# Optimization experiments

Measured on AMD Instinct MI355X. Metric: run time of the kernel, lower is better.

The kernel has to match this reference:

```python
import jax, jax.numpy as jnp
import numpy as np

HEADS = 8
DIM_HEAD = 64
SCALE = DIM_HEAD ** -0.5


def setup_inputs() -> dict:
    key = jax.random.key(0)
    ks = jax.random.split(key, 6)
    b, n, dim, inner = 8, 1024, 512, HEADS * DIM_HEAD
    return {
        "x": jax.random.normal(ks[0], (b, n, dim), jnp.float32),
        "y": jax.random.normal(ks[1], (b, n, dim), jnp.float32),
        "wq": jax.random.normal(ks[2], (dim, inner), jnp.float32) * 0.02,
        "wkv": jax.random.normal(ks[3], (dim, 2 * inner), jnp.float32) * 0.02,
        "wout": jax.random.normal(ks[4], (inner, dim), jnp.float32) * 0.02,
        "bout": jnp.zeros((dim,), jnp.float32),
    }


def _split_heads(t):
    # [b, n, h*d] -> [b, h, n, d]
    b, n, hd = t.shape
    return t.reshape(b, n, HEADS, DIM_HEAD).transpose(0, 2, 1, 3)


def _merge_heads(t):
    # [b, h, n, d] -> [b, n, h*d]
    b, h, n, d = t.shape
    return t.transpose(0, 2, 1, 3).reshape(b, n, h * d)


def _cross_attn(q_in, kv_in, wq, wkv, wout, bout):
    # queries from q_in, keys/values from kv_in; top-(nk//4) masked softmax attention
    nk = kv_in.shape[1]
    q = _split_heads(q_in @ wq)                     # [b,h,nq,d]
    kv = kv_in @ wkv                                # [b,nk,2*inner]
    k, v = jnp.split(kv, 2, axis=-1)
    k, v = _split_heads(k), _split_heads(v)         # [b,h,nk,d]
    dots = jnp.einsum('bhid,bhjd->bhij', q, k) * SCALE  # [b,h,nq,nk]
    kk = max(nk // 4, 1)
    kth = jax.lax.top_k(dots, kk)[0][..., -1:]      # k-th largest per row
    masked = jnp.where(dots >= kth, dots, -jnp.inf)
    attn = jax.nn.softmax(masked, axis=-1)
    out = jnp.einsum('bhij,bhjd->bhid', attn, v)
    return _merge_heads(out) @ wout + bout


def reference(x, y, wq, wkv, wout, bout):
    out_y = _cross_attn(y, x, wq, wkv, wout, bout)  # y attends to x
    out_x = _cross_attn(x, y, wq, wkv, wout, bout)  # x attends to y
    return (out_x, out_y)
```

## Files before the change

kernel.cpp:

```cpp
#include <hip/hip_runtime.h>
#include <hip/hip_bf16.h>

typedef __attribute__((ext_vector_type(8))) short bfx8;
typedef __attribute__((ext_vector_type(4))) float fx4;

__device__ __forceinline__ short f2bf(float f) {
    union { float f; unsigned u; } v; v.f = f;
    unsigned r = v.u + 0x7fffu + ((v.u >> 16) & 1u);
    return (short)(r >> 16);
}
__device__ __forceinline__ float bf2f(short b) {
    union { unsigned u; float f; } v; v.u = ((unsigned)(unsigned short)b) << 16; return v.f;
}

__global__ __launch_bounds__(256) void proj_kernel(
    const float* __restrict__ X, const float* __restrict__ Y,
    const float* __restrict__ wq, const float* __restrict__ wkv,
    short* __restrict__ QpX, short* __restrict__ KpX, short* __restrict__ VbX,
    short* __restrict__ QpY, short* __restrict__ KpY, short* __restrict__ VbY)
{
    const int inp = blockIdx.z;
    const float* A = inp ? Y : X;
    short* Qp = inp ? QpY : QpX;
    short* Kp = inp ? KpY : KpX;
    short* Vb = inp ? VbY : VbX;
    const int mb = blockIdx.x;
    const int nb = blockIdx.y;
    const int tid = threadIdx.x;
    const int lane = tid & 63;
    const int w = tid >> 6, wm = w >> 1, wn = w & 1;
    const int l15 = lane & 15, g8 = (lane >> 4) * 8;

    __shared__ short As[128][72];
    __shared__ short Bs[128][72];

    const float* Bsrc; int ldb, nbase0;
    if (nb < 4) { Bsrc = wq;  ldb = 512;  nbase0 = nb * 128; }
    else        { Bsrc = wkv; ldb = 1024; nbase0 = nb * 128 - 512; }

    fx4 acc[4][4];
    const fx4 z4 = {0.f, 0.f, 0.f, 0.f};
    for (int i = 0; i < 4; i++) for (int j = 0; j < 4; j++) acc[i][j] = z4;

    const int arow = tid >> 1, ahalf = (tid & 1) * 16;
    const int bk = tid >> 3, bnseg = (tid & 7) * 16;

    for (int kb = 0; kb < 512; kb += 32) {
        __syncthreads();
        {
            const float* src = A + (size_t)(mb * 128 + arow) * 512 + kb + ahalf;
            bfx8 h0, h1, l0, l1;
            #pragma unroll
            for (int q = 0; q < 4; q++) {
                float4 v = *(const float4*)(src + q * 4);
                float vv[4] = {v.x, v.y, v.z, v.w};
                #pragma unroll
                for (int c = 0; c < 4; c++) {
                    int idx = q * 4 + c;
                    short h = f2bf(vv[c]);
                    short l = f2bf(vv[c] - bf2f(h));
                    if (idx < 8) { h0[idx] = h; l0[idx] = l; }
                    else         { h1[idx - 8] = h; l1[idx - 8] = l; }
                }
            }
            *(bfx8*)&As[arow][ahalf] = h0;      *(bfx8*)&As[arow][ahalf + 8] = h1;
            *(bfx8*)&As[arow][32 + ahalf] = l0; *(bfx8*)&As[arow][32 + ahalf + 8] = l1;
        }
        {
            const float* src = Bsrc + (size_t)(kb + bk) * ldb + nbase0 + bnseg;
            #pragma unroll
            for (int q = 0; q < 4; q++) {
                float4 v = *(const float4*)(src + q * 4);
                float vv[4] = {v.x, v.y, v.z, v.w};
                #pragma unroll
                for (int c = 0; c < 4; c++) {
                    int n = bnseg + q * 4 + c;
                    short h = f2bf(vv[c]);
                    Bs[n][bk] = h;
                    Bs[n][32 + bk] = f2bf(vv[c] - bf2f(h));
                }
            }
        }
        __syncthreads();
        bfx8 ah[4], al[4], bh[4], bl[4];
        #pragma unroll
        for (int mt = 0; mt < 4; mt++) {
            int r = wm * 64 + mt * 16 + l15;
            ah[mt] = *(bfx8*)&As[r][g8];
            al[mt] = *(bfx8*)&As[r][32 + g8];
        }
        #pragma unroll
        for (int nt = 0; nt < 4; nt++) {
            int r = wn * 64 + nt * 16 + l15;
            bh[nt] = *(bfx8*)&Bs[r][g8];
            bl[nt] = *(bfx8*)&Bs[r][32 + g8];
        }
        #pragma unroll
        for (int mt = 0; mt < 4; mt++)
            #pragma unroll
            for (int nt = 0; nt < 4; nt++) {
                acc[mt][nt] = __builtin_amdgcn_mfma_f32_16x16x32_bf16(ah[mt], bh[nt], acc[mt][nt], 0, 0, 0);
                acc[mt][nt] = __builtin_amdgcn_mfma_f32_16x16x32_bf16(ah[mt], bl[nt], acc[mt][nt], 0, 0, 0);
                acc[mt][nt] = __builtin_amdgcn_mfma_f32_16x16x32_bf16(al[mt], bh[nt], acc[mt][nt], 0, 0, 0);
            }
    }
    #pragma unroll
    for (int mt = 0; mt < 4; mt++)
        #pragma unroll
        for (int nt = 0; nt < 4; nt++)
            #pragma unroll
            for (int r = 0; r < 4; r++) {
                int row = mb * 128 + wm * 64 + mt * 16 + (lane >> 4) * 4 + r;
                int col = nb * 128 + wn * 64 + nt * 16 + l15;
                float v = acc[mt][nt][r];
                int b = row >> 10, n = row & 1023;
                if (col < 512) {
                    v *= 0.125f;
                    int h = col >> 6, d = col & 63;
                    size_t base = ((size_t)(b * 8 + h) * 1024 + n) * 128;
                    short hi = f2bf(v);
                    Qp[base + d] = hi;
                    Qp[base + 64 + d] = f2bf(v - bf2f(hi));
                } else if (col < 1024) {
                    int cc = col - 512;
                    int h = cc >> 6, d = cc & 63;
                    size_t base = ((size_t)(b * 8 + h) * 1024 + n) * 128;
                    short hi = f2bf(v);
                    Kp[base + d] = hi;
                    Kp[base + 64 + d] = f2bf(v - bf2f(hi));
                } else {
                    Vb[(size_t)row * 512 + (col - 1024)] = f2bf(v);
                }
            }
}

__global__ __launch_bounds__(256) void transv_kernel(
    const short* __restrict__ VbX, const short* __restrict__ VbY,
    short* __restrict__ VtX, short* __restrict__ VtY)
{
    const int inp = blockIdx.z;
    const short* Vb = inp ? VbY : VbX;
    short* Vt = inp ? VtY : VtX;
    const int bh = blockIdx.y, b = bh >> 3, h = bh & 7;
    const int nt = blockIdx.x;
    const int tid = threadIdx.x;
    __shared__ short tile[64][66];
    {
        int r = tid >> 2, c0 = (tid & 3) * 16;
        const short* src = Vb + ((size_t)(b * 1024 + nt * 64 + r)) * 512 + h * 64 + c0;
        bfx8 v0 = *(const bfx8*)src;
        bfx8 v1 = *(const bfx8*)(src + 8);
        #pragma unroll
        for (int i = 0; i < 8; i++) { tile[r][c0 + i] = v0[i]; tile[r][c0 + 8 + i] = v1[i]; }
    }
    __syncthreads();
    {
        int d = tid >> 2, n0 = (tid & 3) * 16;
        bfx8 o0, o1;
        #pragma unroll
        for (int i = 0; i < 8; i++) { o0[i] = tile[n0 + i][d]; o1[i] = tile[n0 + 8 + i][d]; }
        short* dst = Vt + ((size_t)(bh * 64 + d)) * 1024 + nt * 64 + n0;
        *(bfx8*)dst = o0;
        *(bfx8*)(dst + 8) = o1;
    }
}

#define PBUF_OFF 0
#define HIST_OFF 65536
#define PMX_OFF  77824
#define PMN_OFF  78336
#define PSUM_OFF 78848
#define RMX_OFF  79360
#define RMN_OFF  79488
#define RT_OFF   79616
#define RB_OFF   79744
#define RN_OFF   79872
#define RC_OFF   80000
#define ATTN_LDS 80128

__global__ __launch_bounds__(512, 4) void attn_kernel(
    const short* __restrict__ QpX, const short* __restrict__ KpX, const short* __restrict__ VtX,
    const short* __restrict__ QpY, const short* __restrict__ KpY, const short* __restrict__ VtY,
    short* __restrict__ inner)
{
    extern __shared__ char smem[];
    unsigned* histU  = (unsigned*)(smem + HIST_OFF);
    float*    candF  = (float*)(smem + HIST_OFF);
    float*    partmx = (float*)(smem + PMX_OFF);
    float*    partmn = (float*)(smem + PMN_OFF);
    float*    partsum= (float*)(smem + PSUM_OFF);
    float*    rowMx  = (float*)(smem + RMX_OFF);
    float*    rowMn  = (float*)(smem + RMN_OFF);
    float*    rowT   = (float*)(smem + RT_OFF);
    int*      rowB   = (int*)(smem + RB_OFF);
    int*      rowNeed= (int*)(smem + RN_OFF);
    int*      rowcnt = (int*)(smem + RC_OFF);

    const int dir = blockIdx.z;
    const short* Qp = dir ? QpY : QpX;
    const short* Kp = dir ? KpX : KpY;
    const short* Vt = dir ? VtX : VtY;
    const int bh = blockIdx.y;
    const int qb = blockIdx.x;
    const int tid = threadIdx.x;
    const int lane = tid & 63;
    const int widx = tid >> 6;
    const int wm = widx >> 2;
    const int ws = widx & 3;
    const int l15 = lane & 15, g = lane >> 4;

    bfx8 qf[2][2];
    {
        const short* qbase = Qp + ((size_t)bh * 1024 + qb * 32 + wm * 16 + l15) * 128;
        #pragma unroll
        for (int ks = 0; ks < 2; ks++)
            #pragma unroll
            for (int p = 0; p < 2; p++)
                qf[ks][p] = *(const bfx8*)(qbase + p * 64 + ks * 32 + g * 8);
    }

    fx4 acc[16];
    {
        const fx4 z4 = {0.f, 0.f, 0.f, 0.f};
        #pragma unroll
        for (int t = 0; t < 16; t++) acc[t] = z4;
        const short* kbase = Kp + ((size_t)bh * 1024 + ws * 256 + l15) * 128 + g * 8;
        #pragma unroll
        for (int t = 0; t < 16; t++) {
            const short* kb = kbase + (size_t)t * 16 * 128;
            bfx8 kh0 = *(const bfx8*)(kb);
            bfx8 kh1 = *(const bfx8*)(kb + 32);
            bfx8 kl0 = *(const bfx8*)(kb + 64);
            bfx8 kl1 = *(const bfx8*)(kb + 96);
            acc[t] = __builtin_amdgcn_mfma_f32_16x16x32_bf16(qf[0][0], kh0, acc[t], 0, 0, 0);
            acc[t] = __builtin_amdgcn_mfma_f32_16x16x32_bf16(qf[0][0], kl0, acc[t], 0, 0, 0);
            acc[t] = __builtin_amdgcn_mfma_f32_16x16x32_bf16(qf[0][1], kh0, acc[t], 0, 0, 0);
            acc[t] = __builtin_amdgcn_mfma_f32_16x16x32_bf16(qf[1][0], kh1, acc[t], 0, 0, 0);
            acc[t] = __builtin_amdgcn_mfma_f32_16x16x32_bf16(qf[1][0], kl1, acc[t], 0, 0, 0);
            acc[t] = __builtin_amdgcn_mfma_f32_16x16x32_bf16(qf[1][1], kh1, acc[t], 0, 0, 0);
        }
    }

    float rmx[4], rmn[4];
    #pragma unroll
    for (int r = 0; r < 4; r++) {
        float a = acc[0][r], b = acc[0][r];
        #pragma unroll
        for (int t = 1; t < 16; t++) { a = fmaxf(a, acc[t][r]); b = fminf(b, acc[t][r]); }
        #pragma unroll
        for (int o = 1; o < 16; o <<= 1) { a = fmaxf(a, __shfl_xor(a, o)); b = fminf(b, __shfl_xor(b, o)); }
        rmx[r] = a; rmn[r] = b;
    }
    if (l15 == 0) {
        #pragma unroll
        for (int r = 0; r < 4; r++) {
            int lrow = wm * 16 + g * 4 + r;
            partmx[lrow * 4 + ws] = rmx[r];
            partmn[lrow * 4 + ws] = rmn[r];
        }
    }
    for (int i = tid; i < 32 * 96; i += 512) histU[i] = 0;
    if (tid < 32) rowcnt[tid] = 0;
    __syncthreads();

    float mxr[4], mnr[4], invr[4];
    #pragma unroll
    for (int r = 0; r < 4; r++) {
        int lrow = wm * 16 + g * 4 + r;
        float a = partmx[lrow * 4 + 0], b = partmn[lrow * 4 + 0];
        #pragma unroll
        for (int j = 1; j < 4; j++) { a = fmaxf(a, partmx[lrow * 4 + j]); b = fminf(b, partmn[lrow * 4 + j]); }
        mxr[r] = a; mnr[r] = b;
        invr[r] = (a - b > 1e-30f) ? 96.0f / (a - b) : 0.0f;
    }
    if (ws == 0 && l15 == 0) {
        #pragma unroll
        for (int r = 0; r < 4; r++) {
            int lrow = wm * 16 + g * 4 + r;
            rowMx[lrow] = mxr[r]; rowMn[lrow] = mnr[r];
        }
    }
    #pragma unroll
    for (int r = 0; r < 4; r++) {
        int lrow = wm * 16 + g * 4 + r;
        #pragma unroll
        for (int t = 0; t < 16; t++) {
            int bin = (int)((acc[t][r] - mnr[r]) * invr[r]);
            bin = bin < 0 ? 0 : (bin > 95 ? 95 : bin);
            atomicAdd(&histU[lrow * 96 + bin], 1u);
        }
    }
    __syncthreads();

    #pragma unroll
    for (int rr = 0; rr < 4; rr++) {
        int row = widx * 4 + rr;
        unsigned c0 = 0, c1 = 0;
        if (lane < 48) { c0 = histU[row * 96 + 2 * lane]; c1 = histU[row * 96 + 2 * lane + 1]; }
        unsigned ts = c0 + c1;
        #pragma unroll
        for (int o = 1; o < 64; o <<= 1) {
            unsigned u = __shfl_down(ts, o);
            if (lane + o < 64) ts += u;
        }
        unsigned ca_lo = ts - c0, ca_hi = ts - c0 - c1;
        bool oklo = (lane < 48) && (ca_lo < 256u) && (ca_lo + c0 >= 256u);
        bool okhi = (lane < 48) && (ca_hi < 256u) && (ca_hi + c1 >= 256u);
        unsigned long long bal = __ballot(oklo || okhi);
        int sl = __ffsll((long long)bal) - 1;
        int myB = oklo ? 2 * lane : 2 * lane + 1;
        int myNeed = 256 - (int)(oklo ? ca_lo : ca_hi);
        int B = __shfl(myB, sl);
        int need = __shfl(myNeed, sl);
        if (lane == 0) {
            float mr = rowMx[row], nr = rowMn[row];
            if (mr - nr < 1e-30f) { rowB[row] = -1; rowT[row] = nr; rowNeed[row] = 1; }
            else { rowB[row] = B; rowNeed[row] = need; }
        }
    }
    __syncthreads();

    #pragma unroll
    for (int r = 0; r < 4; r++) {
        int lrow = wm * 16 + g * 4 + r;
        int B = rowB[lrow];
        #pragma unroll
        for (int t = 0; t < 16; t++) {
            int bin = (int)((acc[t][r] - mnr[r]) * invr[r]);
            bin = bin < 0 ? 0 : (bin > 95 ? 95 : bin);
            if (B >= 0 && bin == B) {
                int idx = atomicAdd(&rowcnt[lrow], 1);
                if (idx < 64) candF[lrow * 64 + idx] = acc[t][r];
            }
        }
    }
    __syncthreads();

    #pragma unroll
    for (int rr = 0; rr < 4; rr++) {
        int row = widx * 4 + rr;
        int B = rowB[row];
        if (B < 0) continue;
        int m = rowcnt[row]; m = m > 64 ? 64 : m;
        int need = rowNeed[row];
        const float* crow = candF + row * 64;
        float v0 = (lane < m) ? crow[lane] : 0.f;
        int cg = 0, ce = 0;
        for (int i = 0; i < m; i++) {
            float c = crow[i];
            cg += (c > v0); ce += (c == v0);
        }
        bool ok = (lane < m) && (cg < need) && (need <= cg + ce);
        unsigned long long bal = __ballot(ok);
        float tt;
        if (bal) tt = __shfl(v0, __ffsll((long long)bal) - 1);
        else     tt = rowMn[row] + (float)B * (rowMx[row] - rowMn[row]) * (1.0f / 96.0f);
        if (lane == 0) rowT[row] = tt;
    }
    __syncthreads();

    #pragma unroll
    for (int r = 0; r < 4; r++) {
        int lrow = wm * 16 + g * 4 + r;
        float tthr = rowT[lrow];
        float s = 0.f;
        unsigned sw = (unsigned)((lrow & 7) << 4);
        #pragma unroll
        for (int t = 0; t < 16; t++) {
            float v = acc[t][r];
            float p = (v >= tthr) ? __expf(v - mxr[r]) : 0.f;
            s += p;
            int col = ws * 256 + t * 16 + l15;
            *(short*)(smem + (size_t)lrow * 2048 + (((unsigned)(col * 2)) ^ sw)) = f2bf(p);
        }
        #pragma unroll
        for (int o = 1; o < 16; o <<= 1) s += __shfl_xor(s, o);
        if (l15 == 0) partsum[lrow * 4 + ws] = s;
    }
    __syncthreads();

    {
        const short* vrow = Vt + ((size_t)bh * 64 + ws * 16 + l15) * 1024;
        const int arow = wm * 16 + l15;
        const unsigned sw = (unsigned)((arow & 7) << 4);
        const char* pbase = smem + (size_t)arow * 2048;
        fx4 acc0 = {0.f, 0.f, 0.f, 0.f}, acc1 = {0.f, 0.f, 0.f, 0.f};
        #pragma unroll
        for (int ks = 0; ks < 32; ks += 2) {
            bfx8 pa0 = *(const bfx8*)(pbase + (((unsigned)(ks * 64 + g * 16)) ^ sw));
            bfx8 vv0 = *(const bfx8*)(vrow + ks * 32 + g * 8);
            bfx8 pa1 = *(const bfx8*)(pbase + (((unsigned)((ks + 1) * 64 + g * 16)) ^ sw));
            bfx8 vv1 = *(const bfx8*)(vrow + (ks + 1) * 32 + g * 8);
            acc0 = __builtin_amdgcn_mfma_f32_16x16x32_bf16(pa0, vv0, acc0, 0, 0, 0);
            acc1 = __builtin_amdgcn_mfma_f32_16x16x32_bf16(pa1, vv1, acc1, 0, 0, 0);
        }
        #pragma unroll
        for (int r = 0; r < 4; r++) {
            int qrow = wm * 16 + g * 4 + r;
            float inv = 1.0f / (partsum[qrow * 4 + 0] + partsum[qrow * 4 + 1] +
                                partsum[qrow * 4 + 2] + partsum[qrow * 4 + 3]);
            float v = (acc0[r] + acc1[r]) * inv;
            size_t orow = (size_t)dir * 8192 + (size_t)(bh >> 3) * 1024 + qb * 32 + qrow;
            inner[orow * 512 + (bh & 7) * 64 + ws * 16 + l15] = f2bf(v);
        }
    }
}

__global__ __launch_bounds__(256) void outproj_kernel(
    const short* __restrict__ inner, const float* __restrict__ wout,
    const float* __restrict__ bout, float* __restrict__ out)
{
    const int mb = blockIdx.x;
    const int nb = blockIdx.y;
    const int tid = threadIdx.x;
    const int lane = tid & 63;
    const int w = tid >> 6, wm = w >> 1, wn = w & 1;
    const int l15 = lane & 15, g8 = (lane >> 4) * 8;

    __shared__ short As[128][40];
    __shared__ short Bs[128][40];

    fx4 acc[4][4];
    const fx4 z4 = {0.f, 0.f, 0.f, 0.f};
    for (int i = 0; i < 4; i++) for (int j = 0; j < 4; j++) acc[i][j] = z4;

    const int arow = tid >> 1, ahalf = (tid & 1) * 16;
    const int bk = tid >> 3, bnseg = (tid & 7) * 16;

    for (int kb = 0; kb < 512; kb += 32) {
        __syncthreads();
        {
            const short* src = inner + (size_t)(mb * 128 + arow) * 512 + kb + ahalf;
            bfx8 v0 = *(const bfx8*)src, v1 = *(const bfx8*)(src + 8);
            *(bfx8*)&As[arow][ahalf] = v0;
            *(bfx8*)&As[arow][ahalf + 8] = v1;
        }
        {
            const float* src = wout + (size_t)(kb + bk) * 512 + nb * 128 + bnseg;
            #pragma unroll
            for (int q = 0; q < 4; q++) {
                float4 v = *(const float4*)(src + q * 4);
                float vv[4] = {v.x, v.y, v.z, v.w};
                #pragma unroll
                for (int c = 0; c < 4; c++) Bs[bnseg + q * 4 + c][bk] = f2bf(vv[c]);
            }
        }
        __syncthreads();
        bfx8 af[4], bf[4];
        #pragma unroll
        for (int mt = 0; mt < 4; mt++) af[mt] = *(bfx8*)&As[wm * 64 + mt * 16 + l15][g8];
        #pragma unroll
        for (int nt = 0; nt < 4; nt++) bf[nt] = *(bfx8*)&Bs[wn * 64 + nt * 16 + l15][g8];
        #pragma unroll
        for (int mt = 0; mt < 4; mt++)
            #pragma unroll
            for (int nt = 0; nt < 4; nt++)
                acc[mt][nt] = __builtin_amdgcn_mfma_f32_16x16x32_bf16(af[mt], bf[nt], acc[mt][nt], 0, 0, 0);
    }
    #pragma unroll
    for (int mt = 0; mt < 4; mt++)
        #pragma unroll
        for (int nt = 0; nt < 4; nt++)
            #pragma unroll
            for (int r = 0; r < 4; r++) {
                int row = mb * 128 + wm * 64 + mt * 16 + (lane >> 4) * 4 + r;
                int col = nb * 128 + wn * 64 + nt * 16 + l15;
                out[(size_t)row * 512 + col] = acc[mt][nt][r] + bout[col];
            }
}

extern "C" void kernel_launch(void* const* d_in, const int* in_sizes, int n_in,
                              void* d_out, int out_size, void* d_ws, size_t ws_size,
                              hipStream_t stream)
{
    const float* x    = (const float*)d_in[0];
    const float* y    = (const float*)d_in[1];
    const float* wq   = (const float*)d_in[2];
    const float* wkv  = (const float*)d_in[3];
    const float* wout = (const float*)d_in[4];
    const float* bout = (const float*)d_in[5];
    float* out = (float*)d_out;

    char* ws = (char*)d_ws;
    size_t off = 0;
    auto alloc = [&](size_t bytes) -> void* {
        void* p = ws + off; off += (bytes + 255) & ~(size_t)255; return p;
    };
    const size_t QP = (size_t)8 * 8 * 1024 * 128 * 2;
    const size_t VB = (size_t)8192 * 512 * 2;
    short* QpX = (short*)alloc(QP);
    short* KpX = (short*)alloc(QP);
    short* QpY = (short*)alloc(QP);
    short* KpY = (short*)alloc(QP);
    short* VbX = (short*)alloc(VB);
    short* VbY = (short*)alloc(VB);
    short* VtX = (short*)alloc(VB);
    short* VtY = (short*)alloc(VB);
    short* inner = (short*)alloc((size_t)2 * 8192 * 512 * 2);
    if (off > ws_size) return;

    proj_kernel<<<dim3(64, 12, 2), 256, 0, stream>>>(x, y, wq, wkv, QpX, KpX, VbX, QpY, KpY, VbY);
    transv_kernel<<<dim3(16, 64, 2), 256, 0, stream>>>(VbX, VbY, VtX, VtY);
    (void)hipFuncSetAttribute((const void*)attn_kernel,
                              hipFuncAttributeMaxDynamicSharedMemorySize, ATTN_LDS);
    attn_kernel<<<dim3(32, 64, 2), 512, ATTN_LDS, stream>>>(QpX, KpX, VtX, QpY, KpY, VtY, inner);
    outproj_kernel<<<dim3(128, 4, 1), 256, 0, stream>>>(inner, wout, bout, out);
}
```

Before: 836.9 us.

## Halve attention query tile to 16 rows, split keys over 8 waves

The attention kernel now handles 16 query rows per block instead of 32. The 8 waves each cover 128 keys, and the PV product is split across two key halves whose partial results are reduced through LDS. LDS use drops from about 80KB to 45KB and per-wave accumulator registers halve, which should allow more resident blocks and more latency hiding. K-fragment loads are also software-prefetched one tile ahead. In exchange, each K/V tile is reloaded for twice as many blocks, and an extra barrier plus partial-sum exchange is added.

Result: faster. 800.3 us (-4.4%).

```diff
diff --git a/kernel.cpp b/kernel.cpp
--- a/kernel.cpp
+++ b/kernel.cpp
@@ -165,18 +165,19 @@
     }
 }
 
-#define PBUF_OFF 0
-#define HIST_OFF 65536
-#define PMX_OFF  77824
-#define PMN_OFF  78336
-#define PSUM_OFF 78848
-#define RMX_OFF  79360
-#define RMN_OFF  79488
-#define RT_OFF   79616
-#define RB_OFF   79744
-#define RN_OFF   79872
-#define RC_OFF   80000
-#define ATTN_LDS 80128
+#define PBUF_BYTES 32768
+#define HIST_OFF   32768
+#define PMX_OFF    38912
+#define PMN_OFF    39424
+#define PSUM_OFF   39936
+#define RMX_OFF    40448
+#define RMN_OFF    40512
+#define RT_OFF     40576
+#define RB_OFF     40640
+#define RN_OFF     40704
+#define RC_OFF     40768
+#define PVP_OFF    40832
+#define ATTN_LDS   44928
 
 __global__ __launch_bounds__(512, 4) void attn_kernel(
     const short* __restrict__ QpX, const short* __restrict__ KpX, const short* __restrict__ VtX,
@@ -195,6 +196,7 @@
     int*      rowB   = (int*)(smem + RB_OFF);
     int*      rowNeed= (int*)(smem + RN_OFF);
     int*      rowcnt = (int*)(smem + RC_OFF);
+    float*    psumPV = (float*)(smem + PVP_OFF);
 
     const int dir = blockIdx.z;
     const short* Qp = dir ? QpY : QpX;
@@ -204,14 +206,12 @@
     const int qb = blockIdx.x;
     const int tid = threadIdx.x;
     const int lane = tid & 63;
-    const int widx = tid >> 6;
-    const int wm = widx >> 2;
-    const int ws = widx & 3;
+    const int w = tid >> 6;
     const int l15 = lane & 15, g = lane >> 4;
 
     bfx8 qf[2][2];
     {
-        const short* qbase = Qp + ((size_t)bh * 1024 + qb * 32 + wm * 16 + l15) * 128;
+        const short* qbase = Qp + ((size_t)bh * 1024 + qb * 16 + l15) * 128;
         #pragma unroll
         for (int ks = 0; ks < 2; ks++)
             #pragma unroll
@@ -219,72 +219,69 @@
                 qf[ks][p] = *(const bfx8*)(qbase + p * 64 + ks * 32 + g * 8);
     }
 
-    fx4 acc[16];
+    fx4 acc[8];
     {
         const fx4 z4 = {0.f, 0.f, 0.f, 0.f};
         #pragma unroll
-        for (int t = 0; t < 16; t++) acc[t] = z4;
-        const short* kbase = Kp + ((size_t)bh * 1024 + ws * 256 + l15) * 128 + g * 8;
-        #pragma unroll
-        for (int t = 0; t < 16; t++) {
-            const short* kb = kbase + (size_t)t * 16 * 128;
-            bfx8 kh0 = *(const bfx8*)(kb);
-            bfx8 kh1 = *(const bfx8*)(kb + 32);
-            bfx8 kl0 = *(const bfx8*)(kb + 64);
-            bfx8 kl1 = *(const bfx8*)(kb + 96);
+        for (int t = 0; t < 8; t++) acc[t] = z4;
+        const short* kbase = Kp + ((size_t)bh * 1024 + w * 128 + l15) * 128 + g * 8;
+        bfx8 kh0 = *(const bfx8*)(kbase);
+        bfx8 kh1 = *(const bfx8*)(kbase + 32);
+        bfx8 kl0 = *(const bfx8*)(kbase + 64);
+        bfx8 kl1 = *(const bfx8*)(kbase + 96);
+        #pragma unroll
+        for (int t = 0; t < 8; t++) {
+            bfx8 nh0, nh1, nl0, nl1;
+            if (t < 7) {
+                const short* nb = kbase + (t + 1) * 2048;
+                nh0 = *(const bfx8*)(nb);
+                nh1 = *(const bfx8*)(nb + 32);
+                nl0 = *(const bfx8*)(nb + 64);
+                nl1 = *(const bfx8*)(nb + 96);
+            }
             acc[t] = __builtin_amdgcn_mfma_f32_16x16x32_bf16(qf[0][0], kh0, acc[t], 0, 0, 0);
             acc[t] = __builtin_amdgcn_mfma_f32_16x16x32_bf16(qf[0][0], kl0, acc[t], 0, 0, 0);
             acc[t] = __builtin_amdgcn_mfma_f32_16x16x32_bf16(qf[0][1], kh0, acc[t], 0, 0, 0);
             acc[t] = __builtin_amdgcn_mfma_f32_16x16x32_bf16(qf[1][0], kh1, acc[t], 0, 0, 0);
             acc[t] = __builtin_amdgcn_mfma_f32_16x16x32_bf16(qf[1][0], kl1, acc[t], 0, 0, 0);
             acc[t] = __builtin_amdgcn_mfma_f32_16x16x32_bf16(qf[1][1], kh1, acc[t], 0, 0, 0);
-        }
-    }
-
-    float rmx[4], rmn[4];
+            kh0 = nh0; kh1 = nh1; kl0 = nl0; kl1 = nl1;
+        }
+    }
+
     #pragma unroll
     for (int r = 0; r < 4; r++) {
         float a = acc[0][r], b = acc[0][r];
         #pragma unroll
-        for (int t = 1; t < 16; t++) { a = fmaxf(a, acc[t][r]); b = fminf(b, acc[t][r]); }
+        for (int t = 1; t < 8; t++) { a = fmaxf(a, acc[t][r]); b = fminf(b, acc[t][r]); }
         #pragma unroll
         for (int o = 1; o < 16; o <<= 1) { a = fmaxf(a, __shfl_xor(a, o)); b = fminf(b, __shfl_xor(b, o)); }
-        rmx[r] = a; rmn[r] = b;
-    }
-    if (l15 == 0) {
-        #pragma unroll
-        for (int r = 0; r < 4; r++) {
-            int lrow = wm * 16 + g * 4 + r;
-            partmx[lrow * 4 + ws] = rmx[r];
-            partmn[lrow * 4 + ws] = rmn[r];
-        }
-    }
-    for (int i = tid; i < 32 * 96; i += 512) histU[i] = 0;
-    if (tid < 32) rowcnt[tid] = 0;
+        if (l15 == 0) {
+            int lrow = g * 4 + r;
+            partmx[lrow * 8 + w] = a;
+            partmn[lrow * 8 + w] = b;
+        }
+    }
+    for (int i = tid; i < 16 * 96; i += 512) histU[i] = 0;
+    if (tid < 16) rowcnt[tid] = 0;
     __syncthreads();
 
     float mxr[4], mnr[4], invr[4];
     #pragma unroll
     for (int r = 0; r < 4; r++) {
-        int lrow = wm * 16 + g * 4 + r;
-        float a = partmx[lrow * 4 + 0], b = partmn[lrow * 4 + 0];
-        #pragma unroll
-        for (int j = 1; j < 4; j++) { a = fmaxf(a, partmx[lrow * 4 + j]); b = fminf(b, partmn[lrow * 4 + j]); }
+        int lrow = g * 4 + r;
+        float a = partmx[lrow * 8 + 0], b = partmn[lrow * 8 + 0];
+        #pragma unroll
+        for (int j = 1; j < 8; j++) { a = fmaxf(a, partmx[lrow * 8 + j]); b = fminf(b, partmn[lrow * 8 + j]); }
         mxr[r] = a; mnr[r] = b;
         invr[r] = (a - b > 1e-30f) ? 96.0f / (a - b) : 0.0f;
-    }
-    if (ws == 0 && l15 == 0) {
-        #pragma unroll
-        for (int r = 0; r < 4; r++) {
-            int lrow = wm * 16 + g * 4 + r;
-            rowMx[lrow] = mxr[r]; rowMn[lrow] = mnr[r];
-        }
+        if (w == 0 && l15 == 0) { rowMx[lrow] = a; rowMn[lrow] = b; }
     }
     #pragma unroll
     for (int r = 0; r < 4; r++) {
-        int lrow = wm * 16 + g * 4 + r;
-        #pragma unroll
-        for (int t = 0; t < 16; t++) {
+        int lrow = g * 4 + r;
+        #pragma unroll
+        for (int t = 0; t < 8; t++) {
             int bin = (int)((acc[t][r] - mnr[r]) * invr[r]);
             bin = bin < 0 ? 0 : (bin > 95 ? 95 : bin);
             atomicAdd(&histU[lrow * 96 + bin], 1u);
@@ -293,8 +290,8 @@
     __syncthreads();
 
     #pragma unroll
-    for (int rr = 0; rr < 4; rr++) {
-        int row = widx * 4 + rr;
+    for (int rr = 0; rr < 2; rr++) {
+        int row = w * 2 + rr;
         unsigned c0 = 0, c1 = 0;
         if (lane < 48) { c0 = histU[row * 96 + 2 * lane]; c1 = histU[row * 96 + 2 * lane + 1]; }
         unsigned ts = c0 + c1;
@@ -322,10 +319,10 @@
 
     #pragma unroll
     for (int r = 0; r < 4; r++) {
-        int lrow = wm * 16 + g * 4 + r;
+        int lrow = g * 4 + r;
         int B = rowB[lrow];
         #pragma unroll
-        for (int t = 0; t < 16; t++) {
+        for (int t = 0; t < 8; t++) {
             int bin = (int)((acc[t][r] - mnr[r]) * invr[r]);
             bin = bin < 0 ? 0 : (bin > 95 ? 95 : bin);
             if (B >= 0 && bin == B) {
@@ -337,8 +334,8 @@
     __syncthreads();
 
     #pragma unroll
-    for (int rr = 0; rr < 4; rr++) {
-        int row = widx * 4 + rr;
+    for (int rr = 0; rr < 2; rr++) {
+        int row = w * 2 + rr;
         int B = rowB[row];
         if (B < 0) continue;
         int m = rowcnt[row]; m = m > 64 ? 64 : m;
@@ -361,47 +358,61 @@
 
     #pragma unroll
     for (int r = 0; r < 4; r++) {
-        int lrow = wm * 16 + g * 4 + r;
+        int lrow = g * 4 + r;
         float tthr = rowT[lrow];
         float s = 0.f;
         unsigned sw = (unsigned)((lrow & 7) << 4);
         #pragma unroll
-        for (int t = 0; t < 16; t++) {
+        for (int t = 0; t < 8; t++) {
             float v = acc[t][r];
             float p = (v >= tthr) ? __expf(v - mxr[r]) : 0.f;
             s += p;
-            int col = ws * 256 + t * 16 + l15;
+            int col = w * 128 + t * 16 + l15;
             *(short*)(smem + (size_t)lrow * 2048 + (((unsigned)(col * 2)) ^ sw)) = f2bf(p);
         }
         #pragma unroll
         for (int o = 1; o < 16; o <<= 1) s += __shfl_xor(s, o);
-        if (l15 == 0) partsum[lrow * 4 + ws] = s;
+        if (l15 == 0) partsum[lrow * 8 + w] = s;
     }
     __syncthreads();
 
     {
-        const short* vrow = Vt + ((size_t)bh * 64 + ws * 16 + l15) * 1024;
-        const int arow = wm * 16 + l15;
-        const unsigned sw = (unsigned)((arow & 7) << 4);
-        const char* pbase = smem + (size_t)arow * 2048;
+        const int ws = w & 3;
+        const int kh = w >> 2;
+        const short* vrow = Vt + ((size_t)bh * 64 + ws * 16 + l15) * 1024 + kh * 512;
+        const char* pbase = smem + (size_t)l15 * 2048;
+        const unsigned sw = (unsigned)((l15 & 7) << 4);
         fx4 acc0 = {0.f, 0.f, 0.f, 0.f}, acc1 = {0.f, 0.f, 0.f, 0.f};
         #pragma unroll
-        for (int ks = 0; ks < 32; ks += 2) {
-            bfx8 pa0 = *(const bfx8*)(pbase + (((unsigned)(ks * 64 + g * 16)) ^ sw));
+        for (int ks = 0; ks < 16; ks += 2) {
+            bfx8 pa0 = *(const bfx8*)(pbase + (((unsigned)(kh * 1024 + ks * 64 + g * 16)) ^ sw));
             bfx8 vv0 = *(const bfx8*)(vrow + ks * 32 + g * 8);
-            bfx8 pa1 = *(const bfx8*)(pbase + (((unsigned)((ks + 1) * 64 + g * 16)) ^ sw));
+            bfx8 pa1 = *(const bfx8*)(pbase + (((unsigned)(kh * 1024 + (ks + 1) * 64 + g * 16)) ^ sw));
             bfx8 vv1 = *(const bfx8*)(vrow + (ks + 1) * 32 + g * 8);
             acc0 = __builtin_amdgcn_mfma_f32_16x16x32_bf16(pa0, vv0, acc0, 0, 0, 0);
             acc1 = __builtin_amdgcn_mfma_f32_16x16x32_bf16(pa1, vv1, acc1, 0, 0, 0);
         }
-        #pragma unroll
-        for (int r = 0; r < 4; r++) {
-            int qrow = wm * 16 + g * 4 + r;
-            float inv = 1.0f / (partsum[qrow * 4 + 0] + partsum[qrow * 4 + 1] +
-                                partsum[qrow * 4 + 2] + partsum[qrow * 4 + 3]);
-            float v = (acc0[r] + acc1[r]) * inv;
-            size_t orow = (size_t)dir * 8192 + (size_t)(bh >> 3) * 1024 + qb * 32 + qrow;
-            inner[orow * 512 + (bh & 7) * 64 + ws * 16 + l15] = f2bf(v);
+        if (kh == 1) {
+            float4 pv;
+            pv.x = acc0[0] + acc1[0]; pv.y = acc0[1] + acc1[1];
+            pv.z = acc0[2] + acc1[2]; pv.w = acc0[3] + acc1[3];
+            *(float4*)&psumPV[(ws * 64 + lane) * 4] = pv;
+        }
+        __syncthreads();
+        if (kh == 0) {
+            const float4 other = *(const float4*)&psumPV[(ws * 64 + lane) * 4];
+            float oth[4] = {other.x, other.y, other.z, other.w};
+            #pragma unroll
+            for (int r = 0; r < 4; r++) {
+                int qrow = g * 4 + r;
+                float denom = partsum[qrow * 8 + 0] + partsum[qrow * 8 + 1] +
+                              partsum[qrow * 8 + 2] + partsum[qrow * 8 + 3] +
+                              partsum[qrow * 8 + 4] + partsum[qrow * 8 + 5] +
+                              partsum[qrow * 8 + 6] + partsum[qrow * 8 + 7];
+                float v = (acc0[r] + acc1[r] + oth[r]) / denom;
+                size_t orow = (size_t)dir * 8192 + (size_t)(bh >> 3) * 1024 + qb * 16 + qrow;
+                inner[orow * 512 + (bh & 7) * 64 + ws * 16 + l15] = f2bf(v);
+            }
         }
     }
 }
@@ -503,6 +514,6 @@
     transv_kernel<<<dim3(16, 64, 2), 256, 0, stream>>>(VbX, VbY, VtX, VtY);
     (void)hipFuncSetAttribute((const void*)attn_kernel,
                               hipFuncAttributeMaxDynamicSharedMemorySize, ATTN_LDS);
-    attn_kernel<<<dim3(32, 64, 2), 512, ATTN_LDS, stream>>>(QpX, KpX, VtX, QpY, KpY, VtY, inner);
+    attn_kernel<<<dim3(64, 64, 2), 512, ATTN_LDS, stream>>>(QpX, KpX, VtX, QpY, KpY, VtY, inner);
     outproj_kernel<<<dim3(128, 4, 1), 256, 0, stream>>>(inner, wout, bout, out);
 }
```
